# Optimization experiments

Measured on AMD Instinct MI355X. Metric: run time of the kernel, lower is better.

The kernel has to match this reference:

```python
import jax, jax.numpy as jnp
import numpy as np

B = 4096
N = 4097  # num_samples; basis fit uses N-1 columns


def _trapz_cumsum(x, t):
    # y[..., 0] = 0; y[..., i] = y[..., i-1] + 0.5*(t[i]-t[i-1])*(x[..., i-1]+x[..., i])
    dt = t[1:] - t[:-1]                                   # (N-1,)
    inc = 0.5 * dt * (x[..., :-1] + x[..., 1:])           # (B,1,N-1)
    zero = jnp.zeros(x.shape[:-1] + (1,), x.dtype)
    return jnp.concatenate([zero, jnp.cumsum(inc, axis=-1)], axis=-1)  # (B,1,N)


def setup_inputs() -> dict:
    key = jax.random.key(0)
    k1, k2 = jax.random.split(key)
    # positive signal so ny + cumsum(x) stays > 0 (needed for pow/log)
    x = jax.random.uniform(k1, (B, 1, N), dtype=jnp.float32, minval=0.1, maxval=1.1)
    # strictly increasing time grid
    dt = jax.random.uniform(k2, (N,), dtype=jnp.float32, minval=1e-3, maxval=1e-2)
    t = jnp.cumsum(dt)
    params = jnp.array([0.5, 1.0], dtype=jnp.float32)  # [r, ny]
    return {"x": x, "t": t, "params": params}


def reference(x, t, params):
    r, ny = params[0], params[1]
    y = _trapz_cumsum(x, t)                  # (B,1,N)
    z = ny + y[:, 0, 1:]                     # (B,N-1)
    phi = jnp.stack([z, z ** r], axis=1)     # (B,2,N-1)  basis matrix
    phip = jnp.linalg.pinv(phi)              # (B,N-1,2)
    x_sl = x[:, :, 1:]                       # (B,1,N-1)
    coeffs = x_sl @ phip                     # (B,1,2)
    x_hat = coeffs @ phi                     # (B,1,N-1)
    res = x_sl - x_hat                       # (B,1,N-1)
    r2 = jnp.sum(res ** 2, axis=-1)          # (B,1)
    return coeffs, x_hat, res, r2
```

## Files before the change

### kernel.cpp

```cpp
#include <hip/hip_runtime.h>

typedef float f32x4 __attribute__((ext_vector_type(4)));

constexpr int NPTS = 4097;
constexpr int M    = 4096;
constexpr int TPB  = 256;
constexpr int NW   = TPB / 64;
constexpr int NJ   = 4;

struct Lds {
    float wt[NW][NJ];
    float gram[NW][6];
};

template<int S>
__device__ __forceinline__ void scan4(const f32x4 a, const f32x4 c,
                                      float d0, float d1, float d2, float d3,
                                      float (&xsj)[4], float (&zlj)[4], float& gsj)
{
    const float m[8] = {a.x, a.y, a.z, a.w, c.x, c.y, c.z, c.w};
    const float x0 = m[S+0], x1 = m[S+1], x2 = m[S+2], x3 = m[S+3], x4 = m[S+4];
    const float i0 = d0 * (x0 + x1);
    const float i1 = d1 * (x1 + x2);
    const float i2 = d2 * (x2 + x3);
    const float i3 = d3 * (x3 + x4);
    zlj[0] = i0;
    zlj[1] = i0 + i1;
    zlj[2] = zlj[1] + i2;
    zlj[3] = zlj[2] + i3;
    gsj = zlj[3];
    xsj[0] = x1; xsj[1] = x2; xsj[2] = x3; xsj[3] = x4;
}

template<int S, bool RHALF>
__device__ __forceinline__ void body(const float* __restrict__ x,
                                     const float* __restrict__ t,
                                     float r, float ny,
                                     float* __restrict__ out,
                                     int b, int B, Lds& L)
{
    const int tid  = threadIdx.x;
    const int lane = tid & 63;
    const int wid  = tid >> 6;

    const float* __restrict__ xal = x + (size_t)b * NPTS - S;

    float xs[NJ][4];
    float zl[NJ][4];
    float gs[NJ];

#pragma unroll
    for (int j = 0; j < NJ; ++j) {
        const int e = j * 1024 + tid * 4;
        const f32x4 a4 = *(const f32x4*)(xal + e);
        const f32x4 c4 = *(const f32x4*)(xal + e + 4);
        const f32x4 tq = *(const f32x4*)(t + e);
        float tn = __shfl_down(tq.x, 1, 64);
        if (lane == 63) tn = t[e + 4];
        const float d0 = 0.5f * (tq.y - tq.x);
        const float d1 = 0.5f * (tq.z - tq.y);
        const float d2 = 0.5f * (tq.w - tq.z);
        const float d3 = 0.5f * (tn   - tq.w);
        scan4<S>(a4, c4, d0, d1, d2, d3, xs[j], zl[j], gs[j]);
    }

    float sc[NJ];
#pragma unroll
    for (int c = 0; c < NJ; ++c) sc[c] = gs[c];
#pragma unroll
    for (int d = 1; d < 64; d <<= 1) {
#pragma unroll
        for (int c = 0; c < NJ; ++c) {
            float u = __shfl_up(sc[c], d, 64);
            if (lane >= d) sc[c] += u;
        }
    }
    if (lane == 63) {
#pragma unroll
        for (int c = 0; c < NJ; ++c) L.wt[wid][c] = sc[c];
    }
    __syncthreads();

    float woff[NJ] = {}, Tt[NJ] = {};
#pragma unroll
    for (int w = 0; w < NW; ++w) {
#pragma unroll
        for (int c = 0; c < NJ; ++c) {
            const float v = L.wt[w][c];
            Tt[c] += v;
            if (w < wid) woff[c] += v;
        }
    }
    float zb[NJ];
    {
        float jacc = 0.f;
#pragma unroll
        for (int j = 0; j < NJ; ++j) {
            zb[j] = ny + jacc + woff[j] + (sc[j] - gs[j]);
            jacc += Tt[j];
        }
    }

    float s0 = 0, s1 = 0, s2 = 0, s3 = 0, s4 = 0, s5 = 0;
#pragma unroll
    for (int j = 0; j < NJ; ++j) {
        float pzz = 0, pzw = 0, pww = 0, pxz = 0, pxw = 0, pxx = 0;
#pragma unroll
        for (int i = 0; i < 4; ++i) {
            const float z = zb[j] + zl[j][i];
            zl[j][i] = z;
            const float w = RHALF ? sqrtf(z) : powf(z, r);
            const float xv = xs[j][i];
            pzz = fmaf(z,  z,  pzz);
            pzw = fmaf(z,  w,  pzw);
            pww = fmaf(w,  w,  pww);
            pxz = fmaf(xv, z,  pxz);
            pxw = fmaf(xv, w,  pxw);
            pxx = fmaf(xv, xv, pxx);
        }
        s0 += pzz; s1 += pzw; s2 += pww; s3 += pxz; s4 += pxw; s5 += pxx;
    }
#pragma unroll
    for (int d = 32; d > 0; d >>= 1) {
        s0 += __shfl_down(s0, d, 64);
        s1 += __shfl_down(s1, d, 64);
        s2 += __shfl_down(s2, d, 64);
        s3 += __shfl_down(s3, d, 64);
        s4 += __shfl_down(s4, d, 64);
        s5 += __shfl_down(s5, d, 64);
    }
    if (lane == 0) {
        L.gram[wid][0] = s0; L.gram[wid][1] = s1; L.gram[wid][2] = s2;
        L.gram[wid][3] = s3; L.gram[wid][4] = s4; L.gram[wid][5] = s5;
    }
    __syncthreads();

    double a0 = 0, a1 = 0, a2 = 0, a3 = 0, a4 = 0, a5 = 0;
#pragma unroll
    for (int w = 0; w < NW; ++w) {
        a0 += L.gram[w][0]; a1 += L.gram[w][1]; a2 += L.gram[w][2];
        a3 += L.gram[w][3]; a4 += L.gram[w][4]; a5 += L.gram[w][5];
    }
    const double det = a0 * a2 - a1 * a1;
    const double inv = 1.0 / det;
    const double c0d = (a3 * a2 - a4 * a1) * inv;
    const double c1d = (a4 * a0 - a3 * a1) * inv;
    const float c0 = (float)c0d;
    const float c1 = (float)c1d;
    if (tid == 0) {
        out[(size_t)b * 2 + 0] = c0;
        out[(size_t)b * 2 + 1] = c1;
        out[(size_t)B * 2 + 2 * (size_t)B * M + b] =
            (float)(a5 - c0d * a3 - c1d * a4);
    }

    float* __restrict__ xhat = out + (size_t)B * 2 + (size_t)b * M;
    float* __restrict__ res  = xhat + (size_t)B * M;

#pragma unroll
    for (int j = 0; j < NJ; ++j) {
        const int e = j * 1024 + tid * 4;
        f32x4 hv, rv;
#pragma unroll
        for (int i = 0; i < 4; ++i) {
            const float z = zl[j][i];
            const float w = RHALF ? sqrtf(z) : powf(z, r);
            const float h  = c0 * z + c1 * w;
            hv[i] = h;
            rv[i] = xs[j][i] - h;
        }
        *(f32x4*)(xhat + e) = hv;
        *(f32x4*)(res  + e) = rv;
    }
}

__global__ __launch_bounds__(TPB)
void vp_kernel(const float* __restrict__ x, const float* __restrict__ t,
               const float* __restrict__ params, float* __restrict__ out, int B)
{
    __shared__ Lds L;
    const float r  = params[0];
    const float ny = params[1];
    const int  b   = blockIdx.x;

    if (r == 0.5f) {
        switch (b & 3) {
        case 0:  body<0, true>(x, t, r, ny, out, b, B, L); break;
        case 1:  body<1, true>(x, t, r, ny, out, b, B, L); break;
        case 2:  body<2, true>(x, t, r, ny, out, b, B, L); break;
        default: body<3, true>(x, t, r, ny, out, b, B, L); break;
        }
    } else {
        switch (b & 3) {
        case 0:  body<0, false>(x, t, r, ny, out, b, B, L); break;
        case 1:  body<1, false>(x, t, r, ny, out, b, B, L); break;
        case 2:  body<2, false>(x, t, r, ny, out, b, B, L); break;
        default: body<3, false>(x, t, r, ny, out, b, B, L); break;
        }
    }
}

extern "C" void kernel_launch(void* const* d_in, const int* in_sizes, int n_in,
                              void* d_out, int out_size, void* d_ws, size_t ws_size,
                              hipStream_t stream) {
    const float* x = (const float*)d_in[0];
    const float* t = (const float*)d_in[1];
    const float* p = (const float*)d_in[2];
    float* out     = (float*)d_out;
    const int B    = in_sizes[0] / NPTS;

    vp_kernel<<<dim3(B), dim3(TPB), 0, stream>>>(x, t, p, out, B);
}
```

Before: 41.69 us.

## Split fused kernel into coefficient pass and emit pass with recomputed scan

Splits the single fused kernel into two launches. The first computes the scan and Gram sums and writes the coefficients. The second re-reads x and t, redoes the scan and writes x_hat and res using coefficients read back from global memory. This drops the second block barrier's wait before the output stores, keeps fewer live registers per kernel, and replaces the t-value shuffle with a direct load. The cost is reading x twice, doing the scan twice, and paying an extra kernel launch.

```diff
diff --git a/kernel.cpp b/kernel.cpp
--- a/kernel.cpp
+++ b/kernel.cpp
@@ -8,22 +8,17 @@
 constexpr int NW   = TPB / 64;
 constexpr int NJ   = 4;
 
-struct Lds {
-    float wt[NW][NJ];
-    float gram[NW][6];
-};
-
 template<int S>
 __device__ __forceinline__ void scan4(const f32x4 a, const f32x4 c,
-                                      float d0, float d1, float d2, float d3,
+                                      const f32x4 tq, float tn,
                                       float (&xsj)[4], float (&zlj)[4], float& gsj)
 {
     const float m[8] = {a.x, a.y, a.z, a.w, c.x, c.y, c.z, c.w};
     const float x0 = m[S+0], x1 = m[S+1], x2 = m[S+2], x3 = m[S+3], x4 = m[S+4];
-    const float i0 = d0 * (x0 + x1);
-    const float i1 = d1 * (x1 + x2);
-    const float i2 = d2 * (x2 + x3);
-    const float i3 = d3 * (x3 + x4);
+    const float i0 = (0.5f * (tq.y - tq.x)) * (x0 + x1);
+    const float i1 = (0.5f * (tq.z - tq.y)) * (x1 + x2);
+    const float i2 = (0.5f * (tq.w - tq.z)) * (x2 + x3);
+    const float i3 = (0.5f * (tn   - tq.w)) * (x3 + x4);
     zlj[0] = i0;
     zlj[1] = i0 + i1;
     zlj[2] = zlj[1] + i2;
@@ -32,36 +27,27 @@
     xsj[0] = x1; xsj[1] = x2; xsj[2] = x3; xsj[3] = x4;
 }
 
-template<int S, bool RHALF>
-__device__ __forceinline__ void body(const float* __restrict__ x,
-                                     const float* __restrict__ t,
-                                     float r, float ny,
-                                     float* __restrict__ out,
-                                     int b, int B, Lds& L)
+template<int S>
+__device__ __forceinline__ void front(const float* __restrict__ x,
+                                      const float* __restrict__ t,
+                                      float ny, int b,
+                                      float (&xs)[NJ][4], float (&zl)[NJ][4],
+                                      float (*wt)[NJ])
 {
     const int tid  = threadIdx.x;
     const int lane = tid & 63;
     const int wid  = tid >> 6;
-
     const float* __restrict__ xal = x + (size_t)b * NPTS - S;
 
-    float xs[NJ][4];
-    float zl[NJ][4];
     float gs[NJ];
-
 #pragma unroll
     for (int j = 0; j < NJ; ++j) {
         const int e = j * 1024 + tid * 4;
         const f32x4 a4 = *(const f32x4*)(xal + e);
         const f32x4 c4 = *(const f32x4*)(xal + e + 4);
         const f32x4 tq = *(const f32x4*)(t + e);
-        float tn = __shfl_down(tq.x, 1, 64);
-        if (lane == 63) tn = t[e + 4];
-        const float d0 = 0.5f * (tq.y - tq.x);
-        const float d1 = 0.5f * (tq.z - tq.y);
-        const float d2 = 0.5f * (tq.w - tq.z);
-        const float d3 = 0.5f * (tn   - tq.w);
-        scan4<S>(a4, c4, d0, d1, d2, d3, xs[j], zl[j], gs[j]);
+        const float tn = t[e + 4];
+        scan4<S>(a4, c4, tq, tn, xs[j], zl[j], gs[j]);
     }
 
     float sc[NJ];
@@ -77,7 +63,7 @@
     }
     if (lane == 63) {
 #pragma unroll
-        for (int c = 0; c < NJ; ++c) L.wt[wid][c] = sc[c];
+        for (int c = 0; c < NJ; ++c) wt[wid][c] = sc[c];
     }
     __syncthreads();
 
@@ -86,20 +72,35 @@
     for (int w = 0; w < NW; ++w) {
 #pragma unroll
         for (int c = 0; c < NJ; ++c) {
-            const float v = L.wt[w][c];
+            const float v = wt[w][c];
             Tt[c] += v;
             if (w < wid) woff[c] += v;
         }
     }
-    float zb[NJ];
-    {
-        float jacc = 0.f;
-#pragma unroll
-        for (int j = 0; j < NJ; ++j) {
-            zb[j] = ny + jacc + woff[j] + (sc[j] - gs[j]);
-            jacc += Tt[j];
-        }
-    }
+    float jacc = 0.f;
+#pragma unroll
+    for (int j = 0; j < NJ; ++j) {
+        const float zb = ny + jacc + woff[j] + (sc[j] - gs[j]);
+        jacc += Tt[j];
+#pragma unroll
+        for (int i = 0; i < 4; ++i) zl[j][i] = zb + zl[j][i];
+    }
+}
+
+template<int S, bool RHALF>
+__device__ __forceinline__ void body1(const float* __restrict__ x,
+                                      const float* __restrict__ t,
+                                      float r, float ny,
+                                      float* __restrict__ out, int b, int B)
+{
+    __shared__ float wt[NW][NJ];
+    __shared__ float gram[NW][6];
+    const int tid  = threadIdx.x;
+    const int lane = tid & 63;
+    const int wid  = tid >> 6;
+
+    float xs[NJ][4], zl[NJ][4];
+    front<S>(x, t, ny, b, xs, zl, wt);
 
     float s0 = 0, s1 = 0, s2 = 0, s3 = 0, s4 = 0, s5 = 0;
 #pragma unroll
@@ -107,9 +108,8 @@
         float pzz = 0, pzw = 0, pww = 0, pxz = 0, pxw = 0, pxx = 0;
 #pragma unroll
         for (int i = 0; i < 4; ++i) {
-            const float z = zb[j] + zl[j][i];
-            zl[j][i] = z;
-            const float w = RHALF ? sqrtf(z) : powf(z, r);
+            const float z  = zl[j][i];
+            const float w  = RHALF ? sqrtf(z) : powf(z, r);
             const float xv = xs[j][i];
             pzz = fmaf(z,  z,  pzz);
             pzw = fmaf(z,  w,  pzw);
@@ -130,29 +130,67 @@
         s5 += __shfl_down(s5, d, 64);
     }
     if (lane == 0) {
-        L.gram[wid][0] = s0; L.gram[wid][1] = s1; L.gram[wid][2] = s2;
-        L.gram[wid][3] = s3; L.gram[wid][4] = s4; L.gram[wid][5] = s5;
+        gram[wid][0] = s0; gram[wid][1] = s1; gram[wid][2] = s2;
+        gram[wid][3] = s3; gram[wid][4] = s4; gram[wid][5] = s5;
     }
     __syncthreads();
 
-    double a0 = 0, a1 = 0, a2 = 0, a3 = 0, a4 = 0, a5 = 0;
-#pragma unroll
-    for (int w = 0; w < NW; ++w) {
-        a0 += L.gram[w][0]; a1 += L.gram[w][1]; a2 += L.gram[w][2];
-        a3 += L.gram[w][3]; a4 += L.gram[w][4]; a5 += L.gram[w][5];
-    }
-    const double det = a0 * a2 - a1 * a1;
-    const double inv = 1.0 / det;
-    const double c0d = (a3 * a2 - a4 * a1) * inv;
-    const double c1d = (a4 * a0 - a3 * a1) * inv;
-    const float c0 = (float)c0d;
-    const float c1 = (float)c1d;
     if (tid == 0) {
-        out[(size_t)b * 2 + 0] = c0;
-        out[(size_t)b * 2 + 1] = c1;
+        double a0 = 0, a1 = 0, a2 = 0, a3 = 0, a4 = 0, a5 = 0;
+#pragma unroll
+        for (int w = 0; w < NW; ++w) {
+            a0 += gram[w][0]; a1 += gram[w][1]; a2 += gram[w][2];
+            a3 += gram[w][3]; a4 += gram[w][4]; a5 += gram[w][5];
+        }
+        const double det = a0 * a2 - a1 * a1;
+        const double inv = 1.0 / det;
+        const double c0d = (a3 * a2 - a4 * a1) * inv;
+        const double c1d = (a4 * a0 - a3 * a1) * inv;
+        out[(size_t)b * 2 + 0] = (float)c0d;
+        out[(size_t)b * 2 + 1] = (float)c1d;
         out[(size_t)B * 2 + 2 * (size_t)B * M + b] =
             (float)(a5 - c0d * a3 - c1d * a4);
     }
+}
+
+__global__ __launch_bounds__(TPB)
+void k_coeff(const float* __restrict__ x, const float* __restrict__ t,
+             const float* __restrict__ params, float* __restrict__ out, int B)
+{
+    const float r  = params[0];
+    const float ny = params[1];
+    const int  b   = blockIdx.x;
+    if (r == 0.5f) {
+        switch (b & 3) {
+        case 0:  body1<0, true>(x, t, r, ny, out, b, B); break;
+        case 1:  body1<1, true>(x, t, r, ny, out, b, B); break;
+        case 2:  body1<2, true>(x, t, r, ny, out, b, B); break;
+        default: body1<3, true>(x, t, r, ny, out, b, B); break;
+        }
+    } else {
+        switch (b & 3) {
+        case 0:  body1<0, false>(x, t, r, ny, out, b, B); break;
+        case 1:  body1<1, false>(x, t, r, ny, out, b, B); break;
+        case 2:  body1<2, false>(x, t, r, ny, out, b, B); break;
+        default: body1<3, false>(x, t, r, ny, out, b, B); break;
+        }
+    }
+}
+
+template<int S, bool RHALF>
+__device__ __forceinline__ void body2(const float* __restrict__ x,
+                                      const float* __restrict__ t,
+                                      float r, float ny,
+                                      float* __restrict__ out, int b, int B)
+{
+    __shared__ float wt[NW][NJ];
+    const int tid = threadIdx.x;
+
+    const float c0 = out[(size_t)b * 2 + 0];
+    const float c1 = out[(size_t)b * 2 + 1];
+
+    float xs[NJ][4], zl[NJ][4];
+    front<S>(x, t, ny, b, xs, zl, wt);
 
     float* __restrict__ xhat = out + (size_t)B * 2 + (size_t)b * M;
     float* __restrict__ res  = xhat + (size_t)B * M;
@@ -165,7 +203,7 @@
         for (int i = 0; i < 4; ++i) {
             const float z = zl[j][i];
             const float w = RHALF ? sqrtf(z) : powf(z, r);
-            const float h  = c0 * z + c1 * w;
+            const float h = c0 * z + c1 * w;
             hv[i] = h;
             rv[i] = xs[j][i] - h;
         }
@@ -175,27 +213,25 @@
 }
 
 __global__ __launch_bounds__(TPB)
-void vp_kernel(const float* __restrict__ x, const float* __restrict__ t,
-               const float* __restrict__ params, float* __restrict__ out, int B)
-{
-    __shared__ Lds L;
+void k_emit(const float* __restrict__ x, const float* __restrict__ t,
+            const float* __restrict__ params, float* __restrict__ out, int B)
+{
     const float r  = params[0];
     const float ny = params[1];
     const int  b   = blockIdx.x;
-
     if (r == 0.5f) {
         switch (b & 3) {
-        case 0:  body<0, true>(x, t, r, ny, out, b, B, L); break;
-        case 1:  body<1, true>(x, t, r, ny, out, b, B, L); break;
-        case 2:  body<2, true>(x, t, r, ny, out, b, B, L); break;
-        default: body<3, true>(x, t, r, ny, out, b, B, L); break;
+        case 0:  body2<0, true>(x, t, r, ny, out, b, B); break;
+        case 1:  body2<1, true>(x, t, r, ny, out, b, B); break;
+        case 2:  body2<2, true>(x, t, r, ny, out, b, B); break;
+        default: body2<3, true>(x, t, r, ny, out, b, B); break;
         }
     } else {
         switch (b & 3) {
-        case 0:  body<0, false>(x, t, r, ny, out, b, B, L); break;
-        case 1:  body<1, false>(x, t, r, ny, out, b, B, L); break;
-        case 2:  body<2, false>(x, t, r, ny, out, b, B, L); break;
-        default: body<3, false>(x, t, r, ny, out, b, B, L); break;
+        case 0:  body2<0, false>(x, t, r, ny, out, b, B); break;
+        case 1:  body2<1, false>(x, t, r, ny, out, b, B); break;
+        case 2:  body2<2, false>(x, t, r, ny, out, b, B); break;
+        default: body2<3, false>(x, t, r, ny, out, b, B); break;
         }
     }
 }
@@ -209,5 +245,6 @@
     float* out     = (float*)d_out;
     const int B    = in_sizes[0] / NPTS;
 
-    vp_kernel<<<dim3(B), dim3(TPB), 0, stream>>>(x, t, p, out, B);
-}
+    k_coeff<<<dim3(B), dim3(TPB), 0, stream>>>(x, t, p, out, B);
+    k_emit <<<dim3(B), dim3(TPB), 0, stream>>>(x, t, p, out, B);
+}
```

After: 61.26 us. +46.9%, slower.

## Process four rows per block with register double-buffered prefetch of next row

Applied to the files above, without the earlier changes.

Each block now handles four consecutive rows. It loads the time-step deltas once and reuses them for all four rows. While computing the current row it prefetches the next row's x values into a second register set, and it double-buffers the LDS scratch so consecutive rows do not conflict. This is meant to hide global load latency and amortize the t loads, at the cost of higher register pressure and a grid that is four times smaller (1024 blocks), which lowers parallelism.

```diff
diff --git a/kernel.cpp b/kernel.cpp
--- a/kernel.cpp
+++ b/kernel.cpp
@@ -7,23 +7,25 @@
 constexpr int TPB  = 256;
 constexpr int NW   = TPB / 64;
 constexpr int NJ   = 4;
+constexpr int RPB  = 4;
 
 struct Lds {
-    float wt[NW][NJ];
-    float gram[NW][6];
+    float wt[2][NW][NJ];
+    float gram[2][NW][6];
 };
 
 template<int S>
 __device__ __forceinline__ void scan4(const f32x4 a, const f32x4 c,
-                                      float d0, float d1, float d2, float d3,
-                                      float (&xsj)[4], float (&zlj)[4], float& gsj)
+                                      const float (&dj)[4],
+                                      float (&xsj)[4], float (&zlj)[4],
+                                      float& gsj)
 {
     const float m[8] = {a.x, a.y, a.z, a.w, c.x, c.y, c.z, c.w};
     const float x0 = m[S+0], x1 = m[S+1], x2 = m[S+2], x3 = m[S+3], x4 = m[S+4];
-    const float i0 = d0 * (x0 + x1);
-    const float i1 = d1 * (x1 + x2);
-    const float i2 = d2 * (x2 + x3);
-    const float i3 = d3 * (x3 + x4);
+    const float i0 = dj[0] * (x0 + x1);
+    const float i1 = dj[1] * (x1 + x2);
+    const float i2 = dj[2] * (x2 + x3);
+    const float i3 = dj[3] * (x3 + x4);
     zlj[0] = i0;
     zlj[1] = i0 + i1;
     zlj[2] = zlj[1] + i2;
@@ -32,52 +34,49 @@
     xsj[0] = x1; xsj[1] = x2; xsj[2] = x3; xsj[3] = x4;
 }
 
-template<int S, bool RHALF>
-__device__ __forceinline__ void body(const float* __restrict__ x,
-                                     const float* __restrict__ t,
-                                     float r, float ny,
-                                     float* __restrict__ out,
-                                     int b, int B, Lds& L)
+template<int R, bool RHALF>
+__device__ __forceinline__ void step(
+    const float* __restrict__ xbase, const float (&d)[NJ][4],
+    float r, float ny, float* __restrict__ out,
+    int b0, int B, Lds& L,
+    f32x4 (&ca)[NJ], f32x4 (&cc)[NJ],
+    f32x4 (&na)[NJ], f32x4 (&nc)[NJ])
 {
     const int tid  = threadIdx.x;
     const int lane = tid & 63;
     const int wid  = tid >> 6;
-
-    const float* __restrict__ xal = x + (size_t)b * NPTS - S;
-
-    float xs[NJ][4];
-    float zl[NJ][4];
-    float gs[NJ];
-
-#pragma unroll
-    for (int j = 0; j < NJ; ++j) {
-        const int e = j * 1024 + tid * 4;
-        const f32x4 a4 = *(const f32x4*)(xal + e);
-        const f32x4 c4 = *(const f32x4*)(xal + e + 4);
-        const f32x4 tq = *(const f32x4*)(t + e);
-        float tn = __shfl_down(tq.x, 1, 64);
-        if (lane == 63) tn = t[e + 4];
-        const float d0 = 0.5f * (tq.y - tq.x);
-        const float d1 = 0.5f * (tq.z - tq.y);
-        const float d2 = 0.5f * (tq.w - tq.z);
-        const float d3 = 0.5f * (tn   - tq.w);
-        scan4<S>(a4, c4, d0, d1, d2, d3, xs[j], zl[j], gs[j]);
-    }
+    const int b    = b0 + R;
+    constexpr int BUF = R & 1;
+
+    if (R < RPB - 1) {
+        const float* __restrict__ nx = xbase + (R + 1) * 4096;
+#pragma unroll
+        for (int j = 0; j < NJ; ++j) {
+            const int e = j * 1024 + tid * 4;
+            na[j] = *(const f32x4*)(nx + e);
+            nc[j] = *(const f32x4*)(nx + e + 4);
+        }
+    }
+
+    float xs[NJ][4], zl[NJ][4], gs[NJ];
+#pragma unroll
+    for (int j = 0; j < NJ; ++j)
+        scan4<R>(ca[j], cc[j], d[j], xs[j], zl[j], gs[j]);
 
     float sc[NJ];
 #pragma unroll
     for (int c = 0; c < NJ; ++c) sc[c] = gs[c];
 #pragma unroll
-    for (int d = 1; d < 64; d <<= 1) {
+    for (int dd = 1; dd < 64; dd <<= 1) {
 #pragma unroll
         for (int c = 0; c < NJ; ++c) {
-            float u = __shfl_up(sc[c], d, 64);
-            if (lane >= d) sc[c] += u;
+            float u = __shfl_up(sc[c], dd, 64);
+            if (lane >= dd) sc[c] += u;
         }
     }
     if (lane == 63) {
 #pragma unroll
-        for (int c = 0; c < NJ; ++c) L.wt[wid][c] = sc[c];
+        for (int c = 0; c < NJ; ++c) L.wt[BUF][wid][c] = sc[c];
     }
     __syncthreads();
 
@@ -86,18 +85,19 @@
     for (int w = 0; w < NW; ++w) {
 #pragma unroll
         for (int c = 0; c < NJ; ++c) {
-            const float v = L.wt[w][c];
+            const float v = L.wt[BUF][w][c];
             Tt[c] += v;
             if (w < wid) woff[c] += v;
         }
     }
-    float zb[NJ];
     {
         float jacc = 0.f;
 #pragma unroll
         for (int j = 0; j < NJ; ++j) {
-            zb[j] = ny + jacc + woff[j] + (sc[j] - gs[j]);
+            const float zb = ny + jacc + woff[j] + (sc[j] - gs[j]);
             jacc += Tt[j];
+#pragma unroll
+            for (int i = 0; i < 4; ++i) zl[j][i] = zb + zl[j][i];
         }
     }
 
@@ -107,9 +107,8 @@
         float pzz = 0, pzw = 0, pww = 0, pxz = 0, pxw = 0, pxx = 0;
 #pragma unroll
         for (int i = 0; i < 4; ++i) {
-            const float z = zb[j] + zl[j][i];
-            zl[j][i] = z;
-            const float w = RHALF ? sqrtf(z) : powf(z, r);
+            const float z  = zl[j][i];
+            const float w  = RHALF ? sqrtf(z) : powf(z, r);
             const float xv = xs[j][i];
             pzz = fmaf(z,  z,  pzz);
             pzw = fmaf(z,  w,  pzw);
@@ -121,25 +120,27 @@
         s0 += pzz; s1 += pzw; s2 += pww; s3 += pxz; s4 += pxw; s5 += pxx;
     }
 #pragma unroll
-    for (int d = 32; d > 0; d >>= 1) {
-        s0 += __shfl_down(s0, d, 64);
-        s1 += __shfl_down(s1, d, 64);
-        s2 += __shfl_down(s2, d, 64);
-        s3 += __shfl_down(s3, d, 64);
-        s4 += __shfl_down(s4, d, 64);
-        s5 += __shfl_down(s5, d, 64);
+    for (int dd = 32; dd > 0; dd >>= 1) {
+        s0 += __shfl_down(s0, dd, 64);
+        s1 += __shfl_down(s1, dd, 64);
+        s2 += __shfl_down(s2, dd, 64);
+        s3 += __shfl_down(s3, dd, 64);
+        s4 += __shfl_down(s4, dd, 64);
+        s5 += __shfl_down(s5, dd, 64);
     }
     if (lane == 0) {
-        L.gram[wid][0] = s0; L.gram[wid][1] = s1; L.gram[wid][2] = s2;
-        L.gram[wid][3] = s3; L.gram[wid][4] = s4; L.gram[wid][5] = s5;
+        L.gram[BUF][wid][0] = s0; L.gram[BUF][wid][1] = s1;
+        L.gram[BUF][wid][2] = s2; L.gram[BUF][wid][3] = s3;
+        L.gram[BUF][wid][4] = s4; L.gram[BUF][wid][5] = s5;
     }
     __syncthreads();
 
     double a0 = 0, a1 = 0, a2 = 0, a3 = 0, a4 = 0, a5 = 0;
 #pragma unroll
     for (int w = 0; w < NW; ++w) {
-        a0 += L.gram[w][0]; a1 += L.gram[w][1]; a2 += L.gram[w][2];
-        a3 += L.gram[w][3]; a4 += L.gram[w][4]; a5 += L.gram[w][5];
+        a0 += L.gram[BUF][w][0]; a1 += L.gram[BUF][w][1];
+        a2 += L.gram[BUF][w][2]; a3 += L.gram[BUF][w][3];
+        a4 += L.gram[BUF][w][4]; a5 += L.gram[BUF][w][5];
     }
     const double det = a0 * a2 - a1 * a1;
     const double inv = 1.0 / det;
@@ -156,7 +157,6 @@
 
     float* __restrict__ xhat = out + (size_t)B * 2 + (size_t)b * M;
     float* __restrict__ res  = xhat + (size_t)B * M;
-
 #pragma unroll
     for (int j = 0; j < NJ; ++j) {
         const int e = j * 1024 + tid * 4;
@@ -165,13 +165,50 @@
         for (int i = 0; i < 4; ++i) {
             const float z = zl[j][i];
             const float w = RHALF ? sqrtf(z) : powf(z, r);
-            const float h  = c0 * z + c1 * w;
+            const float h = c0 * z + c1 * w;
             hv[i] = h;
             rv[i] = xs[j][i] - h;
         }
         *(f32x4*)(xhat + e) = hv;
         *(f32x4*)(res  + e) = rv;
     }
+}
+
+template<bool RHALF>
+__device__ __forceinline__ void run(const float* __restrict__ x,
+                                    const float* __restrict__ t,
+                                    float r, float ny,
+                                    float* __restrict__ out, int B, Lds& L)
+{
+    const int tid = threadIdx.x;
+    const int bid = blockIdx.x;
+    const int b0  = bid * RPB;
+    const float* __restrict__ xbase = x + (size_t)bid * (RPB * NPTS);
+
+    float d[NJ][4];
+#pragma unroll
+    for (int j = 0; j < NJ; ++j) {
+        const int e = j * 1024 + tid * 4;
+        const f32x4 tq = *(const f32x4*)(t + e);
+        const float tn = t[e + 4];
+        d[j][0] = 0.5f * (tq.y - tq.x);
+        d[j][1] = 0.5f * (tq.z - tq.y);
+        d[j][2] = 0.5f * (tq.w - tq.z);
+        d[j][3] = 0.5f * (tn   - tq.w);
+    }
+
+    f32x4 pa[NJ], pc[NJ], qa[NJ], qc[NJ];
+#pragma unroll
+    for (int j = 0; j < NJ; ++j) {
+        const int e = j * 1024 + tid * 4;
+        pa[j] = *(const f32x4*)(xbase + e);
+        pc[j] = *(const f32x4*)(xbase + e + 4);
+    }
+
+    step<0, RHALF>(xbase, d, r, ny, out, b0, B, L, pa, pc, qa, qc);
+    step<1, RHALF>(xbase, d, r, ny, out, b0, B, L, qa, qc, pa, pc);
+    step<2, RHALF>(xbase, d, r, ny, out, b0, B, L, pa, pc, qa, qc);
+    step<3, RHALF>(xbase, d, r, ny, out, b0, B, L, qa, qc, pa, pc);
 }
 
 __global__ __launch_bounds__(TPB)
@@ -181,23 +218,8 @@
     __shared__ Lds L;
     const float r  = params[0];
     const float ny = params[1];
-    const int  b   = blockIdx.x;
-
-    if (r == 0.5f) {
-        switch (b & 3) {
-        case 0:  body<0, true>(x, t, r, ny, out, b, B, L); break;
-        case 1:  body<1, true>(x, t, r, ny, out, b, B, L); break;
-        case 2:  body<2, true>(x, t, r, ny, out, b, B, L); break;
-        default: body<3, true>(x, t, r, ny, out, b, B, L); break;
-        }
-    } else {
-        switch (b & 3) {
-        case 0:  body<0, false>(x, t, r, ny, out, b, B, L); break;
-        case 1:  body<1, false>(x, t, r, ny, out, b, B, L); break;
-        case 2:  body<2, false>(x, t, r, ny, out, b, B, L); break;
-        default: body<3, false>(x, t, r, ny, out, b, B, L); break;
-        }
-    }
+    if (r == 0.5f) run<true >(x, t, r, ny, out, B, L);
+    else           run<false>(x, t, r, ny, out, B, L);
 }
 
 extern "C" void kernel_launch(void* const* d_in, const int* in_sizes, int n_in,
@@ -209,5 +231,5 @@
     float* out     = (float*)d_out;
     const int B    = in_sizes[0] / NPTS;
 
-    vp_kernel<<<dim3(B), dim3(TPB), 0, stream>>>(x, t, p, out, B);
-}
+    vp_kernel<<<dim3(B / RPB), dim3(TPB), 0, stream>>>(x, t, p, out, B);
+}
```

Result: slower. 44.50 us (+6.7%).
